# Kernel optimization log

Measured on AMD Instinct MI355X. Metric: run time of the kernel, lower is better.

Reference implementation:

```python
import jax, jax.numpy as jnp
import numpy as np

D_MODEL = 1024
NUM_HEADS = 8
KEY_DIM = 768      # int(1024*0.75)
VALUE_DIM = 1536   # int(1024*1.5)
HQK = KEY_DIM // NUM_HEADS    # 96
HV = VALUE_DIM // NUM_HEADS   # 192
D_CONV = 4
CHUNK = 64
B, L = 2, 4096


def silu(x):
    return x * jax.nn.sigmoid(x)


def causal_dwconv(x, w):
    # x: (B, L, C), w: (C, K) depthwise kernel; causal (left pad K-1), matches
    # torch Conv1d(padding=K-1) followed by [:, :L] slice.
    K = w.shape[1]
    Lx = x.shape[1]
    xp = jnp.pad(x, ((0, 0), (K - 1, 0), (0, 0)))
    out = xp[:, 0:Lx, :] * w[:, 0]
    for j in range(1, K):
        out = out + xp[:, j:j + Lx, :] * w[:, j]
    return out


def chunk_gated_delta_rule(q, k, v, beta, g, c):
    # q,k: (B,H,L,Dk) L2-normalized; v: (B,H,L,Dv); beta,g: (B,H,L)
    b, h, l, dk = q.shape
    dv = v.shape[-1]
    n = l // c  # L chosen as multiple of chunk size
    q = q * (dk ** -0.5)
    v = v * beta[..., None]
    kb = k * beta[..., None]
    rs = lambda x: x.reshape(b, h, n, c, x.shape[-1])
    q, k, v, kb = rs(q), rs(k), rs(v), rs(kb)
    dec = jnp.cumsum(g.reshape(b, h, n, c), axis=-1)        # (b,h,n,c)
    Lmask = jnp.exp(jnp.minimum(dec[..., :, None] - dec[..., None, :], 0.0))  # (b,h,n,c,c)
    tri_incl = jnp.triu(jnp.ones((c, c), bool))   # upper incl diag -> zeroed
    striu = jnp.triu(jnp.ones((c, c), bool), 1)   # strict upper
    I = jnp.eye(c, dtype=jnp.float32)
    KK = jnp.einsum('bhncd,bhnmd->bhncm', kb, k)  # k_beta @ k^T
    M1 = I + jnp.where(tri_incl, 0.0, KK * Lmask)
    M2 = I + jnp.where(tri_incl, 0.0, KK)
    Ib = jnp.broadcast_to(I, M1.shape)
    solve = lambda M: jax.lax.linalg.triangular_solve(
        M, Ib, left_side=True, lower=True, unit_diagonal=True)
    u_ = solve(M1) @ v       # k_cumsum (= u)
    kcd = solve(M2) @ kb     # k_cumdecay

    def step(S, xs):
        qi, ki, ui, kci, Lmi, di = xs
        ed = jnp.exp(di)[..., None]                 # (b,h,c,1)
        attn = jnp.where(striu, 0.0, jnp.einsum('bhcd,bhmd->bhcm', qi, ki) * Lmi)
        v_new = ui - jnp.einsum('bhcd,bhde->bhce', kci * ed, S)
        oi = jnp.einsum('bhcd,bhde->bhce', qi * ed, S) + attn @ v_new
        dl = di[..., -1]                            # (b,h)
        S = S * jnp.exp(dl)[..., None, None] + jnp.einsum(
            'bhcd,bhce->bhde', ki * jnp.exp(dl[..., None] - di)[..., None], v_new)
        return S, oi

    xs = tuple(jnp.moveaxis(t, 2, 0) for t in (q, k, u_, kcd, Lmask, dec))
    S0 = jnp.zeros((b, h, dk, dv), jnp.float32)
    _, o = jax.lax.scan(step, S0, xs)               # o: (n,b,h,c,dv)
    return jnp.moveaxis(o, 0, 2).reshape(b, h, l, dv)


def setup_inputs() -> dict:
    key = jax.random.key(0)
    ks = jax.random.split(key, 16)
    w = lambda k, shape: (jax.random.normal(k, shape, jnp.float32) * 0.02)
    dt = jnp.exp(jax.random.uniform(ks[10], (NUM_HEADS,)) *
                 (np.log(0.1) - np.log(0.001)) + np.log(0.001))
    dt = jnp.clip(dt, 0.0001, None)
    inv_dt = dt + jnp.log(-jnp.expm1(-dt))
    return {
        'u': jax.random.normal(ks[0], (B, L, D_MODEL), jnp.float32),
        'Wq': w(ks[1], (D_MODEL, KEY_DIM)),
        'Wk': w(ks[2], (D_MODEL, KEY_DIM)),
        'Wv': w(ks[3], (D_MODEL, VALUE_DIM)),
        'Wg': w(ks[4], (D_MODEL, VALUE_DIM)),
        'Wo': w(ks[5], (VALUE_DIM, D_MODEL)),
        'Wgk': w(ks[6], (D_MODEL, NUM_HEADS)),
        'Wb': w(ks[7], (D_MODEL, NUM_HEADS)),
        'b_b': jnp.zeros((NUM_HEADS,), jnp.float32),
        'A_log': jnp.log(jax.random.uniform(ks[8], (NUM_HEADS,), minval=0.001, maxval=16.0)),
        'dt_bias': inv_dt.astype(jnp.float32),
        'conv_q': w(ks[11], (KEY_DIM, D_CONV)) * 10.0,
        'conv_k': w(ks[12], (KEY_DIM, D_CONV)) * 10.0,
        'conv_v': w(ks[13], (VALUE_DIM, D_CONV)) * 10.0,
        'norm_w': jnp.ones((HV,), jnp.float32),
    }


def reference(u, Wq, Wk, Wv, Wg, Wo, Wgk, Wb, b_b, A_log, dt_bias,
              conv_q, conv_k, conv_v, norm_w):
    b, l, _ = u.shape
    q = silu(causal_dwconv(u @ Wq, conv_q))
    k = silu(causal_dwconv(u @ Wk, conv_k))
    v = silu(causal_dwconv(u @ Wv, conv_v))
    gk = u @ Wgk                                    # (B,L,H)
    gk = -jnp.exp(A_log) * jax.nn.softplus(gk + dt_bias)
    gk = gk.transpose(0, 2, 1)                      # (B,H,L)
    beta = jax.nn.sigmoid(u @ Wb + b_b).transpose(0, 2, 1)
    to_bhl = lambda x, d: x.reshape(b, l, NUM_HEADS, d).transpose(0, 2, 1, 3)
    q = to_bhl(q, HQK)
    k = to_bhl(k, HQK)
    v = to_bhl(v, HV)
    l2n = lambda x: x / jnp.maximum(jnp.linalg.norm(x, axis=-1, keepdims=True), 1e-12)
    q, k = l2n(q), l2n(k)
    o = chunk_gated_delta_rule(q, k, v, beta, gk, CHUNK)  # (B,H,L,HV)
    o = o.transpose(0, 2, 1, 3)                     # (B,L,H,HV)
    g = (u @ Wg).reshape(b, l, NUM_HEADS, HV)
    # RMSNormGated, norm_before_gate=True: norm(x)*weight*silu(g)
    on = o * jax.lax.rsqrt(jnp.mean(o * o, axis=-1, keepdims=True) + 1e-5) * norm_w
    on = on * silu(g)
    return on.reshape(b, l, VALUE_DIM) @ Wo
```

## Files before the change

kernel.cpp:

```cpp
#include <hip/hip_runtime.h>

using u16 = unsigned short;
using u32 = unsigned int;
typedef __bf16 bf16x8 __attribute__((ext_vector_type(8)));
typedef u16    u16x8  __attribute__((ext_vector_type(8)));
typedef float  f32x4  __attribute__((ext_vector_type(4)));
typedef float  f32x2  __attribute__((ext_vector_type(2)));
typedef u32    u32x4  __attribute__((ext_vector_type(4)));
typedef u32    u32x2  __attribute__((ext_vector_type(2)));

__device__ __forceinline__ float bf2f(u16 h){ u32 u = ((u32)h)<<16; float f; __builtin_memcpy(&f,&u,4); return f; }
__device__ __forceinline__ u16 f2bf(float f){ u32 u; __builtin_memcpy(&u,&f,4); u32 r = (u + 0x7FFFu + ((u>>16)&1u))>>16; return (u16)r; }
__device__ __forceinline__ float bflo(u32 w){ return bf2f((u16)(w & 0xFFFFu)); }
__device__ __forceinline__ float bfhiw(u32 w){ return bf2f((u16)(w >> 16)); }
__device__ __forceinline__ float sigx(float x){ float e = __expf(-fabsf(x)); float p = 1.f/(1.f+e); return (x>=0.f) ? p : 1.f-p; }

#define BAR_LGKM() asm volatile("s_waitcnt lgkmcnt(0)\n\ts_barrier" ::: "memory")

__device__ __forceinline__ float ldsc(const void* p, size_t i, bool f32){
  return f32 ? ((const float*)p)[i] : bf2f(((const u16*)p)[i]);
}
__device__ __forceinline__ u32x4 ld8bf(const void* p, size_t i, bool f32){
  if (!f32) return *(const u32x4*)((const u16*)p + i);
  const f32x4* q = (const f32x4*)((const float*)p + i);
  f32x4 a = q[0], b = q[1];
  u32x4 r;
  r.x = (u32)f2bf(a.x) | ((u32)f2bf(a.y)<<16);
  r.y = (u32)f2bf(a.z) | ((u32)f2bf(a.w)<<16);
  r.z = (u32)f2bf(b.x) | ((u32)f2bf(b.y)<<16);
  r.w = (u32)f2bf(b.z) | ((u32)f2bf(b.w)<<16);
  return r;
}
__device__ __forceinline__ void unpack8(u32x4 v, float* f){
  f[0]=bflo(v.x); f[1]=bfhiw(v.x); f[2]=bflo(v.y); f[3]=bfhiw(v.y);
  f[4]=bflo(v.z); f[5]=bfhiw(v.z); f[6]=bflo(v.w); f[7]=bfhiw(v.w);
}


__global__ void detect_kernel(const u16* __restrict__ probe, int* __restrict__ flag){
  int t = threadIdx.x;
  int bad = 0;
  for (int i=t; i<1024; i+=64){
    u16 h = probe[i];
    int e = (h>>7)&0xFF;
    if (e >= 0xC0) bad = 1;
  }
  unsigned long long anyb = __ballot(bad);
  if (t==0) *flag = (anyb != 0ull) ? 1 : 0;
}

__global__ void transpose5(const void* __restrict__ Wq, const void* __restrict__ Wk,
                           const void* __restrict__ Wv, const void* __restrict__ Wg,
                           const void* __restrict__ Wo, const void* __restrict__ U,
                           u16* __restrict__ WqT, u16* __restrict__ WkT, u16* __restrict__ WvT,
                           u16* __restrict__ WgT, u16* __restrict__ WoT, u16* __restrict__ ubf,
                           const int* __restrict__ flagp){
  const bool f32 = (*flagp != 0);
  const int bid = blockIdx.x;
  const int t = threadIdx.x;
  if (bid >= 6144){
    size_t base = ((size_t)(bid-6144)*256 + t) * 16;
    u32x4 a = ld8bf(U, base, f32);
    u32x4 b = ld8bf(U, base+8, f32);
    *(u32x4*)(ubf + base)     = a;
    *(u32x4*)(ubf + base + 8) = b;
    return;
  }
  const void* in; u16* out; int C; int local;
  int R;
  if (bid < 768){ in=Wq; out=WqT; R=1024; C=768;  local=bid; }
  else if (bid < 1536){ in=Wk; out=WkT; R=1024; C=768;  local=bid-768; }
  else if (bid < 3072){ in=Wv; out=WvT; R=1024; C=1536; local=bid-1536; }
  else if (bid < 4608){ in=Wg; out=WgT; R=1024; C=1536; local=bid-3072; }
  else { in=Wo; out=WoT; R=1536; C=1024; local=bid-4608; }
  const int nCx = C>>5;
  const int c0 = (local % nCx)*32, r0 = (local / nCx)*32;
  __shared__ u16 tile[32][33];
  int tx = t & 31, ty = t >> 5;
  #pragma unroll
  for (int j=0;j<4;j++){
    int r = r0 + ty + j*8;
    size_t g = (size_t)r*C + c0 + tx;
    tile[ty+j*8][tx] = f32 ? f2bf(((const float*)in)[g]) : ((const u16*)in)[g];
  }
  __syncthreads();
  #pragma unroll
  for (int j=0;j<4;j++){ int c = c0 + ty + j*8; out[(size_t)c*R + r0 + tx] = tile[tx][ty+j*8]; }
}

__global__ __launch_bounds__(256,2) void gemm_bt(const void* __restrict__ A, const u16* __restrict__ Bt,
                                                 void* __restrict__ C, int M, int N, int K,
                                                 const int* __restrict__ flagp, int a_ext, int c_ext,
                                                 int sanitize){
  __shared__ __align__(16) u16 As[128*32];
  __shared__ __align__(16) u16 Bs[128*32];
  const int fl = *flagp;
  const bool af32 = a_ext && fl;
  const bool cf32 = c_ext && fl;
  const int t = threadIdx.x;
  const int bid = blockIdx.x;
  const int nbn = N>>7, rpx = (M>>7)>>3;
  const int x2 = bid & 7, s = bid >> 3;
  const int bm = (x2*rpx + s/nbn)*128;
  const int bn = (s % nbn)*128;
  const int wave = t>>6, lane = t&63, quad = lane>>4, l16 = lane&15;
  const int wm = (wave>>1)*64, wn = (wave&1)*64;
  f32x4 acc[4][4] = {};
  const int row0 = t>>2, kp = (t&3)*8;
  const size_t iA0 = (size_t)(bm+row0)*K + kp;
  const size_t iA1 = iA0 + (size_t)64*K;
  const u16* pB0 = Bt + (size_t)(bn+row0)*K + kp;
  const u16* pB1 = pB0 + (size_t)64*K;
  u32x4 ra0 = ld8bf(A, iA0, af32);
  u32x4 ra1 = ld8bf(A, iA1, af32);
  u32x4 rb0 = *(const u32x4*)pB0;
  u32x4 rb1 = *(const u32x4*)pB1;
  const int nk = K>>5;
  for (int kt=0; kt<nk; ++kt){
    __syncthreads();
    ((u32x4*)As)[t]     = ra0;
    ((u32x4*)As)[t+256] = ra1;
    ((u32x4*)Bs)[t]     = rb0;
    ((u32x4*)Bs)[t+256] = rb1;
    __syncthreads();
    if (kt+1 < nk){
      int o = (kt+1)*32;
      ra0 = ld8bf(A, iA0 + o, af32); ra1 = ld8bf(A, iA1 + o, af32);
      rb0 = *(const u32x4*)(pB0 + o); rb1 = *(const u32x4*)(pB1 + o);
    }
    bf16x8 af[4], bfv[4];
    #pragma unroll
    for (int i=0;i<4;i++){
      af[i]  = *(const bf16x8*)&As[(wm + i*16 + l16)*32 + quad*8];
      bfv[i] = *(const bf16x8*)&Bs[(wn + i*16 + l16)*32 + quad*8];
    }
    #pragma unroll
    for (int i=0;i<4;i++)
      #pragma unroll
      for (int j=0;j<4;j++)
        acc[i][j] = __builtin_amdgcn_mfma_f32_16x16x32_bf16(af[i], bfv[j], acc[i][j], 0,0,0);
  }
  #pragma unroll
  for (int i=0;i<4;i++)
    #pragma unroll
    for (int j=0;j<4;j++)
      #pragma unroll
      for (int r2=0;r2<4;r2++){
        int m = bm + wm + i*16 + quad*4 + r2;
        int n = bn + wn + j*16 + l16;
        float v = acc[i][j][r2];
        if (sanitize && !(v==v && v<1e30f && v>-1e30f)) v = 0.f;
        if (cf32) ((float*)C)[(size_t)m*N + n] = v;
        else      ((u16*)C)[(size_t)m*N + n] = f2bf(v);
      }
}

__global__ __launch_bounds__(256,2) void gemm_qkv(const u16* __restrict__ A,
                                                  const u16* __restrict__ BtQ, const u16* __restrict__ BtK,
                                                  const u16* __restrict__ BtV,
                                                  u16* __restrict__ Cq, u16* __restrict__ Ck, u16* __restrict__ Cv){
  __shared__ __align__(16) u16 As[128*32];
  __shared__ __align__(16) u16 Bs[128*32];
  const int t = threadIdx.x;
  const int bid = blockIdx.x;
  const int x2 = bid & 7, s = bid >> 3;
  const int bm = (x2*8 + s/24)*128;
  const int cgrp = s % 24;
  const u16* Bt; u16* C; int N, bn;
  if (cgrp < 6){ Bt=BtQ; C=Cq; N=768; bn=cgrp*128; }
  else if (cgrp < 12){ Bt=BtK; C=Ck; N=768; bn=(cgrp-6)*128; }
  else { Bt=BtV; C=Cv; N=1536; bn=(cgrp-12)*128; }
  const int K = 1024;
  const int wave = t>>6, lane = t&63, quad = lane>>4, l16 = lane&15;
  const int wm = (wave>>1)*64, wn = (wave&1)*64;
  f32x4 acc[4][4] = {};
  const int row0 = t>>2, kp = (t&3)*8;
  const u16* pA0 = A + (size_t)(bm+row0)*K + kp;
  const u16* pA1 = pA0 + (size_t)64*K;
  const u16* pB0 = Bt + (size_t)(bn+row0)*K + kp;
  const u16* pB1 = pB0 + (size_t)64*K;
  u32x4 ra0 = *(const u32x4*)pA0;
  u32x4 ra1 = *(const u32x4*)pA1;
  u32x4 rb0 = *(const u32x4*)pB0;
  u32x4 rb1 = *(const u32x4*)pB1;
  for (int kt=0; kt<32; ++kt){
    __syncthreads();
    ((u32x4*)As)[t]     = ra0;
    ((u32x4*)As)[t+256] = ra1;
    ((u32x4*)Bs)[t]     = rb0;
    ((u32x4*)Bs)[t+256] = rb1;
    __syncthreads();
    if (kt+1 < 32){
      int o = (kt+1)*32;
      ra0 = *(const u32x4*)(pA0 + o); ra1 = *(const u32x4*)(pA1 + o);
      rb0 = *(const u32x4*)(pB0 + o); rb1 = *(const u32x4*)(pB1 + o);
    }
    bf16x8 af[4], bfv[4];
    #pragma unroll
    for (int i=0;i<4;i++){
      af[i]  = *(const bf16x8*)&As[(wm + i*16 + l16)*32 + quad*8];
      bfv[i] = *(const bf16x8*)&Bs[(wn + i*16 + l16)*32 + quad*8];
    }
    #pragma unroll
    for (int i=0;i<4;i++)
      #pragma unroll
      for (int j=0;j<4;j++)
        acc[i][j] = __builtin_amdgcn_mfma_f32_16x16x32_bf16(af[i], bfv[j], acc[i][j], 0,0,0);
  }
  #pragma unroll
  for (int i=0;i<4;i++)
    #pragma unroll
    for (int j=0;j<4;j++)
      #pragma unroll
      for (int r2=0;r2<4;r2++){
        int m = bm + wm + i*16 + quad*4 + r2;
        int n = bn + wn + j*16 + l16;
        C[(size_t)m*N + n] = f2bf(acc[i][j][r2]);
      }
}

__global__ __launch_bounds__(384) void prep_kernel(
    const void* __restrict__ u, const void* __restrict__ Wgk, const void* __restrict__ Wb,
    const void* __restrict__ b_b, const void* __restrict__ A_log, const void* __restrict__ dt_b,
    const u16* __restrict__ qraw, const u16* __restrict__ kraw, const u16* __restrict__ vraw,
    const void* __restrict__ cq, const void* __restrict__ ck, const void* __restrict__ cv,
    float* __restrict__ gk, float* __restrict__ beta,
    u16* __restrict__ qn, u16* __restrict__ kn, u16* __restrict__ vb,
    const int* __restrict__ flagp){
  const bool f32 = (*flagp != 0);
  const int bl = blockIdx.x;
  const int b = bl>>12, l = bl&4095;
  const int t = threadIdx.x;
  __shared__ float red[4][16];
  __shared__ float sqP[96], skP[96];
  __shared__ float nrmq[8], nrmk[8];
  __shared__ float bS2[8];

  if (t < 256){
    float accg[8] = {0,0,0,0,0,0,0,0};
    float accb[8] = {0,0,0,0,0,0,0,0};
    for (int d=t; d<1024; d+=256){
      float uv = ldsc(u, (size_t)bl*1024 + d, f32);
      u32x4 wg = ld8bf(Wgk, (size_t)d*8, f32);
      u32x4 wb = ld8bf(Wb,  (size_t)d*8, f32);
      accg[0] += uv*bflo(wg.x); accg[1] += uv*bfhiw(wg.x);
      accg[2] += uv*bflo(wg.y); accg[3] += uv*bfhiw(wg.y);
      accg[4] += uv*bflo(wg.z); accg[5] += uv*bfhiw(wg.z);
      accg[6] += uv*bflo(wg.w); accg[7] += uv*bfhiw(wg.w);
      accb[0] += uv*bflo(wb.x); accb[1] += uv*bfhiw(wb.x);
      accb[2] += uv*bflo(wb.y); accb[3] += uv*bfhiw(wb.y);
      accb[4] += uv*bflo(wb.z); accb[5] += uv*bfhiw(wb.z);
      accb[6] += uv*bflo(wb.w); accb[7] += uv*bfhiw(wb.w);
    }
    #pragma unroll
    for (int h=0;h<8;h++){
      #pragma unroll
      for (int off=32; off>=1; off>>=1){
        accg[h] += __shfl_down(accg[h], off);
        accb[h] += __shfl_down(accb[h], off);
      }
    }
    int wv = t>>6, lane = t&63;
    if (lane==0){
      #pragma unroll
      for (int h=0;h<8;h++){ red[wv][h]=accg[h]; red[wv][8+h]=accb[h]; }
    }
  }
  __syncthreads();
  if (t<16){
    float sum = red[0][t]+red[1][t]+red[2][t]+red[3][t];
    if (t<8){
      int h=t;
      float x = sum + ldsc(dt_b, h, f32);
      float sp = (x>20.f) ? x : log1pf(__expf(x));
      gk[(size_t)(b*8+h)*4096 + l] = -__expf(ldsc(A_log, h, f32)) * sp;
    } else {
      int h=t-8;
      float x = sum + ldsc(b_b, h, f32);
      float bv = sigx(x);
      beta[(size_t)(b*8+h)*4096 + l] = bv;
      bS2[h] = bv;
    }
  }
  __syncthreads();

  const int base = b*4096;
  int role, c0;
  if (t < 96){ role=0; c0=t*8; }
  else if (t < 192){ role=1; c0=(t-96)*8; }
  else { role=2; c0=(t-192)*8; }
  const u16* raw = (role==0)? qraw : (role==1)? kraw : vraw;
  const void* cw = (role==0)? cq : (role==1)? ck : cv;
  const int C = (role==2)? 1536 : 768;

  float w[8][4];
  #pragma unroll
  for (int g=0; g<4; g++){
    u32x4 W = ld8bf(cw, (size_t)c0*4 + g*8, f32);
    w[g*2+0][0]=bflo(W.x); w[g*2+0][1]=bfhiw(W.x); w[g*2+0][2]=bflo(W.y); w[g*2+0][3]=bfhiw(W.y);
    w[g*2+1][0]=bflo(W.z); w[g*2+1][1]=bfhiw(W.z); w[g*2+1][2]=bflo(W.w); w[g*2+1][3]=bfhiw(W.w);
  }
  float acc[8];
  #pragma unroll
  for (int ch=0; ch<8; ch++) acc[ch] = 0.f;
  #pragma unroll
  for (int j=0;j<4;j++){
    if (l >= 3-j){
      u32x4 iv = *(const u32x4*)(raw + (size_t)(base+l-3+j)*C + c0);
      float in[8]; unpack8(iv, in);
      #pragma unroll
      for (int ch=0;ch<8;ch++) acc[ch] += in[ch]*w[ch][j];
    }
  }
  #pragma unroll
  for (int ch=0;ch<8;ch++) acc[ch] = acc[ch]*sigx(acc[ch]);

  if (role==2){
    int h = c0/192, d0 = c0 - h*192;
    float bv = bS2[h];
    u32x4 pv;
    pv.x = (u32)f2bf(acc[0]*bv) | ((u32)f2bf(acc[1]*bv)<<16);
    pv.y = (u32)f2bf(acc[2]*bv) | ((u32)f2bf(acc[3]*bv)<<16);
    pv.z = (u32)f2bf(acc[4]*bv) | ((u32)f2bf(acc[5]*bv)<<16);
    pv.w = (u32)f2bf(acc[6]*bv) | ((u32)f2bf(acc[7]*bv)<<16);
    *(u32x4*)&vb[((size_t)(b*8+h)*4096 + l)*192 + d0] = pv;
  } else {
    float ss = 0.f;
    #pragma unroll
    for (int ch=0;ch<8;ch++) ss += acc[ch]*acc[ch];
    if (role==0) sqP[t] = ss; else skP[t-96] = ss;
  }
  __syncthreads();
  if (t < 8){
    float s = 0.f;
    #pragma unroll
    for (int j=0;j<12;j++) s += sqP[t*12+j];
    nrmq[t] = fmaxf(sqrtf(s), 1e-12f);
  } else if (t < 16){
    int h = t-8;
    float s = 0.f;
    #pragma unroll
    for (int j=0;j<12;j++) s += skP[h*12+j];
    nrmk[h] = fmaxf(sqrtf(s), 1e-12f);
  }
  __syncthreads();
  if (role==0){
    int h = c0/96, d0 = c0 - h*96;
    float nr = nrmq[h];
    float v0 = acc[0]/nr*0.10206207261596575f, v1 = acc[1]/nr*0.10206207261596575f;
    float v2 = acc[2]/nr*0.10206207261596575f, v3 = acc[3]/nr*0.10206207261596575f;
    float v4 = acc[4]/nr*0.10206207261596575f, v5 = acc[5]/nr*0.10206207261596575f;
    float v6 = acc[6]/nr*0.10206207261596575f, v7 = acc[7]/nr*0.10206207261596575f;
    u32x4 pv;
    pv.x = (u32)f2bf(v0) | ((u32)f2bf(v1)<<16);
    pv.y = (u32)f2bf(v2) | ((u32)f2bf(v3)<<16);
    pv.z = (u32)f2bf(v4) | ((u32)f2bf(v5)<<16);
    pv.w = (u32)f2bf(v6) | ((u32)f2bf(v7)<<16);
    *(u32x4*)&qn[((size_t)(b*8+h)*4096 + l)*96 + d0] = pv;
  } else if (role==1){
    int h = c0/96, d0 = c0 - h*96;
    float nr = nrmk[h];
    u32x4 pv;
    pv.x = (u32)f2bf(acc[0]/nr*1.0f) | ((u32)f2bf(acc[1]/nr*1.0f)<<16);
    pv.y = (u32)f2bf(acc[2]/nr*1.0f) | ((u32)f2bf(acc[3]/nr*1.0f)<<16);
    pv.z = (u32)f2bf(acc[4]/nr*1.0f) | ((u32)f2bf(acc[5]/nr*1.0f)<<16);
    pv.w = (u32)f2bf(acc[6]/nr*1.0f) | ((u32)f2bf(acc[7]/nr*1.0f)<<16);
    *(u32x4*)&kn[((size_t)(b*8+h)*4096 + l)*96 + d0] = pv;
  }
}

__global__ __launch_bounds__(320,2) void chunkprep_kernel(
    const u16* __restrict__ qn, u16* __restrict__ knw, const u16* __restrict__ vb,
    const float* __restrict__ beta, const float* __restrict__ gk,
    u16* __restrict__ attn, u16* __restrict__ kcd, u16* __restrict__ uA,
    float* __restrict__ edG, float* __restrict__ aG){
  __shared__ __align__(16) u16 kS[64*104];
  __shared__ __align__(16) u16 qS[64*104];
  __shared__ float M1[64*64];
  __shared__ float M2[64*64];
  __shared__ float bS[64], dS[64], wS2[64];
  const int t = threadIdx.x;
  const int bhn = blockIdx.x;
  const size_t rowb = (size_t)bhn*64;
  const int w = t>>6, l = t&63, l16 = l&15, quad = l>>4;

  #pragma unroll
  for (int j=0;j<3;j++){
    int v = t + 320*j;
    if (v < 768){
      int rr = v/12, c8 = v - rr*12;
      size_t g = (rowb+rr)*96 + c8*8;
      *(u32x4*)&kS[rr*104 + c8*8] = *(const u32x4*)(knw + g);
      *(u32x4*)&qS[rr*104 + c8*8] = *(const u32x4*)(qn + g);
    }
  }
  if (t<64){
    bS[t] = beta[rowb+t];
    float g = gk[rowb+t];
    #pragma unroll
    for (int off=1; off<64; off<<=1){
      float xx = __shfl_up(g, off);
      if (t >= off) g += xx;
    }
    dS[t] = g;
    float dl = __shfl(g, 63);
    edG[rowb+t] = __expf(g);
    wS2[t] = __expf(dl - g);
    if (t==0) aG[bhn] = __expf(dl);
  }
  __syncthreads();

  for (int idx=t; idx<6144; idx+=320){
    int d = idx>>6, ll = idx&63;
    knw[(size_t)bhn*6144 + idx] = f2bf(bf2f(kS[ll*104 + d])*wS2[ll]);
  }

  float x[64];
  const int mode0 = (t<192) ? 0 : 1;
  const int c0 = (t<192) ? t : (t-192);
  const bool active = (t < 288);
  if (active){
    if (mode0==0){
      #pragma unroll
      for (int i=0;i<64;i++) x[i] = bf2f(vb[(rowb+i)*192 + c0]);
    } else {
      #pragma unroll
      for (int i=0;i<64;i++) x[i] = bS[i]*bf2f(kS[i*104 + c0]);
    }
  }

  if (t < 256){
    bf16x8 qA[3], kA[3];
    #pragma unroll
    for (int ks=0;ks<3;ks++){
      qA[ks] = *(const bf16x8*)&qS[(w*16+l16)*104 + ks*32 + quad*8];
      kA[ks] = *(const bf16x8*)&kS[(w*16+l16)*104 + ks*32 + quad*8];
    }
    const size_t ab = (size_t)bhn*4096;
    #pragma unroll
    for (int nt=0;nt<4;nt++){
      f32x4 aQ = {0.f,0.f,0.f,0.f}, aK = {0.f,0.f,0.f,0.f};
      #pragma unroll
      for (int ks=0;ks<3;ks++){
        bf16x8 Bf = *(const bf16x8*)&kS[(nt*16+l16)*104 + ks*32 + quad*8];
        aQ = __builtin_amdgcn_mfma_f32_16x16x32_bf16(qA[ks], Bf, aQ,0,0,0);
        aK = __builtin_amdgcn_mfma_f32_16x16x32_bf16(kA[ks], Bf, aK,0,0,0);
      }
      #pragma unroll
      for (int r=0;r<4;r++){
        int row = w*16 + quad*4 + r;
        int col = nt*16 + l16;
        float lm = __expf(fminf(dS[row]-dS[col], 0.f));
        attn[ab + row*64 + col] = (col<=row) ? f2bf(aQ[r]*lm) : (u16)0;
        if (col<row){
          float kkb = aK[r]*bS[row];
          M2[row*64+col] = kkb;
          M1[row*64+col] = kkb*lm;
        }
      }
    }
  }
  __syncthreads();

  if (active){
    const float* Mb = (mode0==0) ? M1 : M2;
    #pragma unroll
    for (int i=1;i<64;i++){
      float acc = x[i];
      #pragma unroll
      for (int m=0;m<i;m++) acc -= Mb[i*64+m]*x[m];
      x[i] = acc;
    }
    if (mode0==0){
      #pragma unroll
      for (int i=0;i<64;i++) uA[(rowb+i)*192 + c0] = f2bf(x[i]);
    } else {
      #pragma unroll
      for (int i=0;i<64;i++) kcd[(rowb+i)*96 + c0] = f2bf(x[i]);
    }
  }
}

__global__ __launch_bounds__(256,1) void scan_glin_kernel(
    const u16* __restrict__ qn, const u16* __restrict__ kTw, const u16* __restrict__ kcd,
    const u16* __restrict__ attn, const u16* __restrict__ uA,
    const float* __restrict__ edG, const float* __restrict__ aG,
    u16* __restrict__ o,
    const u16* __restrict__ Ag, const u16* __restrict__ Btg,
    u16* __restrict__ Cg0, u16* __restrict__ Cg1, u16* __restrict__ Cg2, u16* __restrict__ Cg3){
  __shared__ __align__(16) char smem[16640];
  const int bid = blockIdx.x;
  const int t = threadIdx.x;

  if (bid >= 192){
    u16* As = (u16*)smem;
    u16* Bs = (u16*)(smem + 8192);
    const int j = bid - 192;
    const int x2 = j & 7, s = j >> 3;
    const int bm = (x2*8 + s/12)*128;
    const int bn = (s % 12)*128;
    const int wave = t>>6, lane = t&63, quad = lane>>4, l16 = lane&15;
    const int wm = (wave>>1)*64, wn = (wave&1)*64;
    f32x4 acc[4][4] = {};
    const int row0 = t>>2, kp = (t&3)*8;
    const u16* pA0 = Ag + (size_t)(bm+row0)*1024 + kp;
    const u16* pA1 = pA0 + (size_t)64*1024;
    const u16* pB0 = Btg + (size_t)(bn+row0)*1024 + kp;
    const u16* pB1 = pB0 + (size_t)64*1024;
    u32x4 ra0 = *(const u32x4*)pA0;
    u32x4 ra1 = *(const u32x4*)pA1;
    u32x4 rb0 = *(const u32x4*)pB0;
    u32x4 rb1 = *(const u32x4*)pB1;
    for (int kt=0; kt<32; ++kt){
      __syncthreads();
      ((u32x4*)As)[t]     = ra0;
      ((u32x4*)As)[t+256] = ra1;
      ((u32x4*)Bs)[t]     = rb0;
      ((u32x4*)Bs)[t+256] = rb1;
      __syncthreads();
      if (kt+1 < 32){
        int o2 = (kt+1)*32;
        ra0 = *(const u32x4*)(pA0 + o2); ra1 = *(const u32x4*)(pA1 + o2);
        rb0 = *(const u32x4*)(pB0 + o2); rb1 = *(const u32x4*)(pB1 + o2);
      }
      bf16x8 af[4], bfv[4];
      #pragma unroll
      for (int i=0;i<4;i++){
        af[i]  = *(const bf16x8*)&As[(wm + i*16 + l16)*32 + quad*8];
        bfv[i] = *(const bf16x8*)&Bs[(wn + i*16 + l16)*32 + quad*8];
      }
      #pragma unroll
      for (int i=0;i<4;i++)
        #pragma unroll
        for (int j2=0;j2<4;j2++)
          acc[i][j2] = __builtin_amdgcn_mfma_f32_16x16x32_bf16(af[i], bfv[j2], acc[i][j2], 0,0,0);
    }
    u16* Cp; int mo;
    if (bm < 5376){ Cp = Cg0; mo = bm; }
    else if (bm < 6656){ Cp = Cg1; mo = bm - 5376; }
    else if (bm < 7680){ Cp = Cg2; mo = bm - 6656; }
    else { Cp = Cg3; mo = bm - 7680; }
    #pragma unroll
    for (int i=0;i<4;i++)
      #pragma unroll
      for (int j2=0;j2<4;j2++)
        #pragma unroll
        for (int r2=0;r2<4;r2++){
          int m = mo + wm + i*16 + quad*4 + r2;
          int n = bn + wn + j2*16 + l16;
          Cp[(size_t)m*1536 + n] = f2bf(acc[i][j2][r2]);
        }
    return;
  }

  __builtin_amdgcn_s_setprio(1);
  const int bh = bid % 16, eg = bid / 16;
  const int e0 = eg*16;
  const int w = t>>6, l = t&63, l16 = l&15, quad = l>>4;

  u16* vnewT = (u16*)smem;
  u16* Sbf   = (u16*)(smem + 2304);

  for (int i=t; i<16*104; i+=256) Sbf[i] = 0;

  size_t rowb = (size_t)bh*4096;
  size_t ab   = (size_t)bh*64*4096;

  u32x4 kcdF[3], qF[3], attF[2]; u16 uF[4];
  u32x4 kuC[2][2], kuN[2][2];
  auto pfAB = [&](size_t rowbN){
    #pragma unroll
    for (int ks=0; ks<3; ks++){
      size_t gg = (rowbN + w*16 + l16)*96 + ks*32 + quad*8;
      kcdF[ks] = *(const u32x4*)(kcd + gg);
      qF[ks]   = *(const u32x4*)(qn + gg);
    }
  };
  auto pfATT = [&](size_t abN){
    #pragma unroll
    for (int ks=0; ks<2; ks++)
      attF[ks] = *(const u32x4*)(attn + abN + (w*16 + l16)*64 + ks*32 + quad*8);
  };
  auto pfU = [&](size_t rowbN){
    #pragma unroll
    for (int r=0;r<4;r++)
      uF[r] = uA[(rowbN + w*16 + quad*4 + r)*192 + e0 + l16];
  };
  auto pfKU = [&](size_t chunkIdx, u32x4 (&dst)[2][2]){
    #pragma unroll
    for (int i=0;i<2;i++){
      int tid = w + 4*i;
      if (tid < 6){
        size_t base = chunkIdx*6144 + (size_t)(tid*16 + l16)*64 + quad*8;
        dst[i][0] = *(const u32x4*)(kTw + base);
        dst[i][1] = *(const u32x4*)(kTw + base + 32);
      }
    }
  };

  pfAB(rowb); pfU(rowb); pfATT(ab);
  pfKU(rowb>>6, kuC);
  f32x4 edC = *(const f32x4*)&edG[rowb + w*16 + quad*4];
  float aexpC = aG[rowb>>6];
  __syncthreads();
  f32x4 Sreg[2] = {};

  for (int n=0;n<64;n++){
    const size_t rowbN = rowb + 64;
    const size_t abN = ab + 4096;
    f32x4 edN = {0.f,0.f,0.f,0.f};
    float aexpN = 0.f;
    if (n<63){
      pfKU(rowbN>>6, kuN);
      edN = *(const f32x4*)&edG[rowbN + w*16 + quad*4];
      aexpN = aG[rowbN>>6];
    }
    f32x4 accA = {0.f,0.f,0.f,0.f}, accQ = {0.f,0.f,0.f,0.f};
    #pragma unroll
    for (int ks=0;ks<3;ks++){
      bf16x8 Bf = *(const bf16x8*)&Sbf[l16*104 + ks*32 + quad*8];
      accA = __builtin_amdgcn_mfma_f32_16x16x32_bf16(*(const bf16x8*)&kcdF[ks], Bf, accA,0,0,0);
      accQ = __builtin_amdgcn_mfma_f32_16x16x32_bf16(*(const bf16x8*)&qF[ks],  Bf, accQ,0,0,0);
    }
    #pragma unroll
    for (int r=0;r<4;r++){
      float vn = bf2f(uF[r]) - edC[r]*accA[r];
      vnewT[l16*72 + (w*16+quad*4+r)] = f2bf(vn);
      accQ[r] *= edC[r];
    }
    if (n<63){ pfAB(rowbN); pfU(rowbN); }
    BAR_LGKM();
    #pragma unroll
    for (int ks=0;ks<2;ks++){
      bf16x8 Bv = *(const bf16x8*)&vnewT[l16*72 + ks*32 + quad*8];
      accQ = __builtin_amdgcn_mfma_f32_16x16x32_bf16(*(const bf16x8*)&attF[ks], Bv, accQ,0,0,0);
    }
    #pragma unroll
    for (int r=0;r<4;r++)
      o[(rowb + w*16 + quad*4 + r)*192 + e0 + l16] = f2bf(accQ[r]);
    if (n<63) pfATT(abN);
    #pragma unroll
    for (int i=0;i<2;i++){
      int tid = w + 4*i;
      if (tid < 6){
        int mt = tid;
        f32x4 acc = (f32x4){0.f,0.f,0.f,0.f};
        #pragma unroll
        for (int ks=0;ks<2;ks++){
          bf16x8 Bv = *(const bf16x8*)&vnewT[l16*72 + ks*32 + quad*8];
          acc = __builtin_amdgcn_mfma_f32_16x16x32_bf16(*(const bf16x8*)&kuC[i][ks], Bv, acc,0,0,0);
        }
        f32x4 ns;
        ns.x = Sreg[i].x*aexpC + acc.x;
        ns.y = Sreg[i].y*aexpC + acc.y;
        ns.z = Sreg[i].z*aexpC + acc.z;
        ns.w = Sreg[i].w*aexpC + acc.w;
        Sreg[i] = ns;
        u32x2 pv;
        pv.x = (u32)f2bf(ns.x) | ((u32)f2bf(ns.y)<<16);
        pv.y = (u32)f2bf(ns.z) | ((u32)f2bf(ns.w)<<16);
        *(u32x2*)&Sbf[l16*104 + mt*16 + quad*4] = pv;
      }
    }
    BAR_LGKM();
    rowb = rowbN; ab = abN;
    edC = edN; aexpC = aexpN;
    kuC[0][0]=kuN[0][0]; kuC[0][1]=kuN[0][1]; kuC[1][0]=kuN[1][0]; kuC[1][1]=kuN[1][1];
  }
}

__global__ __launch_bounds__(192) void epilogue_kernel(const u16* __restrict__ o,
                                                       const u16* __restrict__ g0, const u16* __restrict__ g1,
                                                       const u16* __restrict__ g2, const u16* __restrict__ g3,
                                                       const void* __restrict__ nw, u16* __restrict__ on,
                                                       const int* __restrict__ flagp){
  const bool f32 = (*flagp != 0);
  const int bl = blockIdx.x;
  const int t = threadIdx.x;
  const int b = bl>>12, l = bl&4095;
  const int h = t/24, d0 = (t - h*24)*8;
  __shared__ float part[192];
  __shared__ float rsS[8];
  u32x4 ov = *(const u32x4*)&o[((size_t)(b*8+h)*4096 + l)*192 + d0];
  float x[8]; unpack8(ov, x);
  float ss = 0.f;
  #pragma unroll
  for (int ch=0;ch<8;ch++) ss += x[ch]*x[ch];
  part[t] = ss;
  __syncthreads();
  if (t < 8){
    float s = 0.f;
    #pragma unroll
    for (int j=0;j<24;j++) s += part[t*24+j];
    rsS[t] = rsqrtf(s/192.f + 1e-5f);
  }
  __syncthreads();
  float rs = rsS[h];
  const u16* gp; int bo;
  if (bl < 5376){ gp = g0; bo = bl; }
  else if (bl < 6656){ gp = g1; bo = bl - 5376; }
  else if (bl < 7680){ gp = g2; bo = bl - 6656; }
  else { gp = g3; bo = bl - 7680; }
  u32x4 gv = *(const u32x4*)&gp[(size_t)bo*1536 + h*192 + d0];
  float gf[8]; unpack8(gv, gf);
  u32x4 nv = ld8bf(nw, d0, f32);
  float nf[8]; unpack8(nv, nf);
  u32x4 pv;
  float r[8];
  #pragma unroll
  for (int ch=0;ch<8;ch++) r[ch] = x[ch]*rs*nf[ch]*gf[ch]*sigx(gf[ch]);
  pv.x = (u32)f2bf(r[0]) | ((u32)f2bf(r[1])<<16);
  pv.y = (u32)f2bf(r[2]) | ((u32)f2bf(r[3])<<16);
  pv.z = (u32)f2bf(r[4]) | ((u32)f2bf(r[5])<<16);
  pv.w = (u32)f2bf(r[6]) | ((u32)f2bf(r[7])<<16);
  *(u32x4*)&on[(size_t)bl*1536 + h*192 + d0] = pv;
}

extern "C" void kernel_launch(void* const* d_in, const int* in_sizes, int n_in,
                              void* d_out, int out_size, void* d_ws, size_t ws_size,
                              hipStream_t stream){
  (void)in_sizes; (void)n_in; (void)out_size; (void)ws_size;
  const void* u     = d_in[0];
  const void* Wq    = d_in[1];
  const void* Wk    = d_in[2];
  const void* Wv    = d_in[3];
  const void* Wg    = d_in[4];
  const void* Wo    = d_in[5];
  const void* Wgk   = d_in[6];
  const void* Wb    = d_in[7];
  const void* b_b   = d_in[8];
  const void* A_log = d_in[9];
  const void* dt_b  = d_in[10];
  const void* cq    = d_in[11];
  const void* ck    = d_in[12];
  const void* cv    = d_in[13];
  const void* nw    = d_in[14];

  char* w = (char*)d_ws;
  size_t off = 0;
  auto take = [&](size_t bytes)->char*{
    char* p = w + off;
    off += (bytes + 255) & ~(size_t)255;
    return p;
  };
  int* flag = (int*)take(256);
  u16* WqT  = (u16*)take((size_t)768*1024*2);
  u16* WkT  = (u16*)take((size_t)768*1024*2);
  u16* WvT  = (u16*)take((size_t)1536*1024*2);
  u16* WgT  = (u16*)take((size_t)1536*1024*2);
  u16* WoT  = (u16*)take((size_t)1024*1536*2);
  u16* qraw = (u16*)take((size_t)8192*768*2);
  u16* kraw = (u16*)take((size_t)8192*768*2);
  u16* vraw = (u16*)take((size_t)8192*1536*2);
  u16* qn   = (u16*)take((size_t)8192*768*2);
  u16* kn   = (u16*)take((size_t)8192*768*2);
  u16* vb   = (u16*)take((size_t)8192*1536*2);
  u16* ubf  = (u16*)take((size_t)8192*1024*2);
  float* gkA   = (float*)WqT;
  float* betaA = gkA + 65536;
  float* edG   = betaA + 65536;
  float* wGA   = edG + 65536;
  float* aGA   = wGA + 65536;
  u16* attnA = qraw;
  u16* kcdA  = kraw;
  u16* uuA   = vraw;
  u16* oA    = vb;
  u16* onA   = vraw;
  u16* glin0 = (u16*)d_out;
  u16* glin1 = attnA + (size_t)1024*64*64;
  u16* glin2 = WvT;
  u16* glin3 = WkT;

  detect_kernel<<<1,64,0,stream>>>((const u16*)u, flag);
  transpose5<<<8192,256,0,stream>>>(Wq, Wk, Wv, Wg, Wo, u,
                                    WqT, WkT, WvT, WgT, WoT, ubf, flag);
  gemm_qkv<<<1536,256,0,stream>>>(ubf, WqT, WkT, WvT, qraw, kraw, vraw);
  prep_kernel<<<8192,384,0,stream>>>(u, Wgk, Wb, b_b, A_log, dt_b,
                                     qraw, kraw, vraw, cq, ck, cv,
                                     gkA, betaA, qn, kn, vb, flag);
  chunkprep_kernel<<<1024,320,0,stream>>>(qn, kn, vb, betaA, gkA, attnA, kcdA, uuA,
                                          edG, aGA);
  scan_glin_kernel<<<960,256,0,stream>>>(qn, kn , kcdA, attnA, uuA, edG, aGA, oA,
                                         ubf, WgT, glin0, glin1, glin2, glin3);
  epilogue_kernel<<<8192,192,0,stream>>>(oA, glin0, glin1, glin2, glin3, nw, onA, flag);
  gemm_bt<<<512,256,0,stream>>>(onA, WoT, d_out, 8192, 1024, 1536, flag, 0, 1, 1);
}
```

Before: 559.8 us.

## Move gate/beta projections from prep kernel into extra blocks of QKV GEMM

The per-token gk and beta projections (u @ Wgk, u @ Wb with softplus/sigmoid) move out of prep_kernel into 8192 extra blocks appended to the gemm_qkv grid. Those blocks can run alongside the GEMM tiles, and prep_kernel no longer does the reduction and its extra barriers before the conv work. The projection loop is also specialised per input dtype to avoid conversion overhead. gk/beta/edG/aGA now get dedicated workspace buffers instead of aliasing WqT, which the GEMM still reads while the new blocks write. The added blocks raise gemm_qkv's launch size and may compete with GEMM tiles for occupancy.

```diff
diff --git a/kernel.cpp b/kernel.cpp
--- a/kernel.cpp
+++ b/kernel.cpp
@@ -158,11 +158,85 @@
 __global__ __launch_bounds__(256,2) void gemm_qkv(const u16* __restrict__ A,
                                                   const u16* __restrict__ BtQ, const u16* __restrict__ BtK,
                                                   const u16* __restrict__ BtV,
-                                                  u16* __restrict__ Cq, u16* __restrict__ Ck, u16* __restrict__ Cv){
+                                                  u16* __restrict__ Cq, u16* __restrict__ Ck, u16* __restrict__ Cv,
+                                                  const void* __restrict__ u, const void* __restrict__ Wgk,
+                                                  const void* __restrict__ Wb, const void* __restrict__ b_b,
+                                                  const void* __restrict__ A_log, const void* __restrict__ dt_b,
+                                                  float* __restrict__ gk, float* __restrict__ beta,
+                                                  const int* __restrict__ flagp){
   __shared__ __align__(16) u16 As[128*32];
   __shared__ __align__(16) u16 Bs[128*32];
+  __shared__ float red[4][16];
   const int t = threadIdx.x;
   const int bid = blockIdx.x;
+
+  if (bid >= 1536){
+    const bool f32 = (*flagp != 0);
+    const int bl = bid - 1536;
+    const int b2 = bl>>12, l = bl&4095;
+    float accg[8] = {0,0,0,0,0,0,0,0};
+    float accb[8] = {0,0,0,0,0,0,0,0};
+    if (f32){
+      const float* uf  = (const float*)u + (size_t)bl*1024;
+      const float* wgf = (const float*)Wgk;
+      const float* wbf = (const float*)Wb;
+      for (int d=t; d<1024; d+=256){
+        float uv = uf[d];
+        f32x4 ga = *(const f32x4*)(wgf + (size_t)d*8);
+        f32x4 gb = *(const f32x4*)(wgf + (size_t)d*8 + 4);
+        f32x4 ba = *(const f32x4*)(wbf + (size_t)d*8);
+        f32x4 bb = *(const f32x4*)(wbf + (size_t)d*8 + 4);
+        accg[0] += uv*ga.x; accg[1] += uv*ga.y; accg[2] += uv*ga.z; accg[3] += uv*ga.w;
+        accg[4] += uv*gb.x; accg[5] += uv*gb.y; accg[6] += uv*gb.z; accg[7] += uv*gb.w;
+        accb[0] += uv*ba.x; accb[1] += uv*ba.y; accb[2] += uv*ba.z; accb[3] += uv*ba.w;
+        accb[4] += uv*bb.x; accb[5] += uv*bb.y; accb[6] += uv*bb.z; accb[7] += uv*bb.w;
+      }
+    } else {
+      const u16* uh = (const u16*)u + (size_t)bl*1024;
+      for (int d=t; d<1024; d+=256){
+        float uv = bf2f(uh[d]);
+        u32x4 wg = *(const u32x4*)((const u16*)Wgk + (size_t)d*8);
+        u32x4 wb = *(const u32x4*)((const u16*)Wb  + (size_t)d*8);
+        accg[0] += uv*bflo(wg.x); accg[1] += uv*bfhiw(wg.x);
+        accg[2] += uv*bflo(wg.y); accg[3] += uv*bfhiw(wg.y);
+        accg[4] += uv*bflo(wg.z); accg[5] += uv*bfhiw(wg.z);
+        accg[6] += uv*bflo(wg.w); accg[7] += uv*bfhiw(wg.w);
+        accb[0] += uv*bflo(wb.x); accb[1] += uv*bfhiw(wb.x);
+        accb[2] += uv*bflo(wb.y); accb[3] += uv*bfhiw(wb.y);
+        accb[4] += uv*bflo(wb.z); accb[5] += uv*bfhiw(wb.z);
+        accb[6] += uv*bflo(wb.w); accb[7] += uv*bfhiw(wb.w);
+      }
+    }
+    #pragma unroll
+    for (int h=0;h<8;h++){
+      #pragma unroll
+      for (int off=32; off>=1; off>>=1){
+        accg[h] += __shfl_down(accg[h], off);
+        accb[h] += __shfl_down(accb[h], off);
+      }
+    }
+    int wv = t>>6, lane = t&63;
+    if (lane==0){
+      #pragma unroll
+      for (int h=0;h<8;h++){ red[wv][h]=accg[h]; red[wv][8+h]=accb[h]; }
+    }
+    __syncthreads();
+    if (t<16){
+      float sum = red[0][t]+red[1][t]+red[2][t]+red[3][t];
+      if (t<8){
+        int h=t;
+        float x = sum + ldsc(dt_b, h, f32);
+        float sp = (x>20.f) ? x : log1pf(__expf(x));
+        gk[(size_t)(b2*8+h)*4096 + l] = -__expf(ldsc(A_log, h, f32)) * sp;
+      } else {
+        int h=t-8;
+        float x = sum + ldsc(b_b, h, f32);
+        beta[(size_t)(b2*8+h)*4096 + l] = sigx(x);
+      }
+    }
+    return;
+  }
+
   const int x2 = bid & 7, s = bid >> 3;
   const int bm = (x2*8 + s/24)*128;
   const int cgrp = s % 24;
@@ -220,69 +294,20 @@
 }
 
 __global__ __launch_bounds__(384) void prep_kernel(
-    const void* __restrict__ u, const void* __restrict__ Wgk, const void* __restrict__ Wb,
-    const void* __restrict__ b_b, const void* __restrict__ A_log, const void* __restrict__ dt_b,
     const u16* __restrict__ qraw, const u16* __restrict__ kraw, const u16* __restrict__ vraw,
     const void* __restrict__ cq, const void* __restrict__ ck, const void* __restrict__ cv,
-    float* __restrict__ gk, float* __restrict__ beta,
+    const float* __restrict__ beta,
     u16* __restrict__ qn, u16* __restrict__ kn, u16* __restrict__ vb,
     const int* __restrict__ flagp){
   const bool f32 = (*flagp != 0);
   const int bl = blockIdx.x;
   const int b = bl>>12, l = bl&4095;
   const int t = threadIdx.x;
-  __shared__ float red[4][16];
   __shared__ float sqP[96], skP[96];
   __shared__ float nrmq[8], nrmk[8];
   __shared__ float bS2[8];
 
-  if (t < 256){
-    float accg[8] = {0,0,0,0,0,0,0,0};
-    float accb[8] = {0,0,0,0,0,0,0,0};
-    for (int d=t; d<1024; d+=256){
-      float uv = ldsc(u, (size_t)bl*1024 + d, f32);
-      u32x4 wg = ld8bf(Wgk, (size_t)d*8, f32);
-      u32x4 wb = ld8bf(Wb,  (size_t)d*8, f32);
-      accg[0] += uv*bflo(wg.x); accg[1] += uv*bfhiw(wg.x);
-      accg[2] += uv*bflo(wg.y); accg[3] += uv*bfhiw(wg.y);
-      accg[4] += uv*bflo(wg.z); accg[5] += uv*bfhiw(wg.z);
-      accg[6] += uv*bflo(wg.w); accg[7] += uv*bfhiw(wg.w);
-      accb[0] += uv*bflo(wb.x); accb[1] += uv*bfhiw(wb.x);
-      accb[2] += uv*bflo(wb.y); accb[3] += uv*bfhiw(wb.y);
-      accb[4] += uv*bflo(wb.z); accb[5] += uv*bfhiw(wb.z);
-      accb[6] += uv*bflo(wb.w); accb[7] += uv*bfhiw(wb.w);
-    }
-    #pragma unroll
-    for (int h=0;h<8;h++){
-      #pragma unroll
-      for (int off=32; off>=1; off>>=1){
-        accg[h] += __shfl_down(accg[h], off);
-        accb[h] += __shfl_down(accb[h], off);
-      }
-    }
-    int wv = t>>6, lane = t&63;
-    if (lane==0){
-      #pragma unroll
-      for (int h=0;h<8;h++){ red[wv][h]=accg[h]; red[wv][8+h]=accb[h]; }
-    }
-  }
-  __syncthreads();
-  if (t<16){
-    float sum = red[0][t]+red[1][t]+red[2][t]+red[3][t];
-    if (t<8){
-      int h=t;
-      float x = sum + ldsc(dt_b, h, f32);
-      float sp = (x>20.f) ? x : log1pf(__expf(x));
-      gk[(size_t)(b*8+h)*4096 + l] = -__expf(ldsc(A_log, h, f32)) * sp;
-    } else {
-      int h=t-8;
-      float x = sum + ldsc(b_b, h, f32);
-      float bv = sigx(x);
-      beta[(size_t)(b*8+h)*4096 + l] = bv;
-      bS2[h] = bv;
-    }
-  }
-  __syncthreads();
+  if (t<8) bS2[t] = beta[(size_t)(b*8+t)*4096 + l];
 
   const int base = b*4096;
   int role, c0;
@@ -315,6 +340,7 @@
   #pragma unroll
   for (int ch=0;ch<8;ch++) acc[ch] = acc[ch]*sigx(acc[ch]);
 
+  __syncthreads();
   if (role==2){
     int h = c0/192, d0 = c0 - h*192;
     float bv = bS2[h];
@@ -347,15 +373,11 @@
   if (role==0){
     int h = c0/96, d0 = c0 - h*96;
     float nr = nrmq[h];
-    float v0 = acc[0]/nr*0.10206207261596575f, v1 = acc[1]/nr*0.10206207261596575f;
-    float v2 = acc[2]/nr*0.10206207261596575f, v3 = acc[3]/nr*0.10206207261596575f;
-    float v4 = acc[4]/nr*0.10206207261596575f, v5 = acc[5]/nr*0.10206207261596575f;
-    float v6 = acc[6]/nr*0.10206207261596575f, v7 = acc[7]/nr*0.10206207261596575f;
     u32x4 pv;
-    pv.x = (u32)f2bf(v0) | ((u32)f2bf(v1)<<16);
-    pv.y = (u32)f2bf(v2) | ((u32)f2bf(v3)<<16);
-    pv.z = (u32)f2bf(v4) | ((u32)f2bf(v5)<<16);
-    pv.w = (u32)f2bf(v6) | ((u32)f2bf(v7)<<16);
+    pv.x = (u32)f2bf(acc[0]/nr*0.10206207261596575f) | ((u32)f2bf(acc[1]/nr*0.10206207261596575f)<<16);
+    pv.y = (u32)f2bf(acc[2]/nr*0.10206207261596575f) | ((u32)f2bf(acc[3]/nr*0.10206207261596575f)<<16);
+    pv.z = (u32)f2bf(acc[4]/nr*0.10206207261596575f) | ((u32)f2bf(acc[5]/nr*0.10206207261596575f)<<16);
+    pv.w = (u32)f2bf(acc[6]/nr*0.10206207261596575f) | ((u32)f2bf(acc[7]/nr*0.10206207261596575f)<<16);
     *(u32x4*)&qn[((size_t)(b*8+h)*4096 + l)*96 + d0] = pv;
   } else if (role==1){
     int h = c0/96, d0 = c0 - h*96;
@@ -756,11 +778,10 @@
   u16* kn   = (u16*)take((size_t)8192*768*2);
   u16* vb   = (u16*)take((size_t)8192*1536*2);
   u16* ubf  = (u16*)take((size_t)8192*1024*2);
-  float* gkA   = (float*)WqT;
-  float* betaA = gkA + 65536;
-  float* edG   = betaA + 65536;
-  float* wGA   = edG + 65536;
-  float* aGA   = wGA + 65536;
+  float* gkA   = (float*)take(65536*4);
+  float* betaA = (float*)take(65536*4);
+  float* edG   = (float*)take(65536*4);
+  float* aGA   = (float*)take(1024*4);
   u16* attnA = qraw;
   u16* kcdA  = kraw;
   u16* uuA   = vraw;
@@ -774,10 +795,10 @@
   detect_kernel<<<1,64,0,stream>>>((const u16*)u, flag);
   transpose5<<<8192,256,0,stream>>>(Wq, Wk, Wv, Wg, Wo, u,
                                     WqT, WkT, WvT, WgT, WoT, ubf, flag);
-  gemm_qkv<<<1536,256,0,stream>>>(ubf, WqT, WkT, WvT, qraw, kraw, vraw);
-  prep_kernel<<<8192,384,0,stream>>>(u, Wgk, Wb, b_b, A_log, dt_b,
-                                     qraw, kraw, vraw, cq, ck, cv,
-                                     gkA, betaA, qn, kn, vb, flag);
+  gemm_qkv<<<9728,256,0,stream>>>(ubf, WqT, WkT, WvT, qraw, kraw, vraw,
+                                  u, Wgk, Wb, b_b, A_log, dt_b, gkA, betaA, flag);
+  prep_kernel<<<8192,384,0,stream>>>(qraw, kraw, vraw, cq, ck, cv, betaA,
+                                     qn, kn, vb, flag);
   chunkprep_kernel<<<1024,320,0,stream>>>(qn, kn, vb, betaA, gkA, attnA, kcdA, uuA,
                                           edG, aGA);
   scan_glin_kernel<<<960,256,0,stream>>>(qn, kn , kcdA, attnA, uuA, edG, aGA, oA,
```

New measurement: 543.1 us. 3.0% less time.
